# Performance work log

Measured on AMD Instinct MI355X. Metric: run time of the kernel, lower is better.

Reference implementation:

```python
import jax, jax.numpy as jnp
import numpy as np

B, T, D, H, A = 1, 262144, 8, 64, 4  # batch, seq_len, state_dim, hidden, n_actions


def setup_inputs() -> dict:
    key = jax.random.key(0)
    ks = jax.random.split(key, 10)
    s = lambda k, shape, sc: jax.random.normal(k, shape, dtype=jnp.float32) * sc
    return {
        "x": jax.random.normal(ks[0], (B, T, D), dtype=jnp.float32),
        # encoder MLP (Dense->tanh, Dense->tanh)
        "W1": s(ks[1], (D, H), 0.5), "b1": jnp.zeros((H,), jnp.float32),
        "W2": s(ks[2], (H, H), 0.15), "b2": jnp.zeros((H,), jnp.float32),
        # SimpleRNN params: h_t = tanh(x_t @ Wx + h_{t-1} @ Wh + b_rnn)
        "Wx": s(ks[3], (H, H), 0.15), "Wh": s(ks[4], (H, H), 0.1),
        "b_rnn": jnp.zeros((H,), jnp.float32),
        # means head
        "Wm": s(ks[5], (H, A), 0.01), "bm": jnp.zeros((A,), jnp.float32),
    }


def reference(x, W1, b1, W2, b2, Wx, Wh, b_rnn, Wm, bm):
    # Masking(mask_value=0): a timestep is masked if ALL features == 0
    mask = jnp.any(x != 0.0, axis=-1)  # [B, T] bool
    # TimeDistributed encoder (applies pointwise over time -> plain batched matmul)
    h1 = jnp.tanh(x @ W1 + b1)          # [B, T, H]
    h2 = jnp.tanh(h1 @ W2 + b2)         # [B, T, H]
    # Precompute input contribution to the RNN outside the scan (efficient form)
    xz = h2 @ Wx + b_rnn                # [B, T, H]

    def step(h, inp):
        z, m = inp                       # z: [B, H], m: [B]
        h_new = jnp.tanh(z + h @ Wh)
        # masked timesteps: carry previous state through (Keras RNN masking semantics)
        h = jnp.where(m[:, None], h_new, h)
        return h, h

    h0 = jnp.zeros((B, H), x.dtype)
    _, hs = jax.lax.scan(step, h0, (jnp.swapaxes(xz, 0, 1), jnp.swapaxes(mask, 0, 1)))
    hs = jnp.swapaxes(hs, 0, 1)          # [B, T, H]
    means = hs @ Wm + bm                 # [B, T, A]
    return means
```

## Files before the change

### kernel.cpp

```cpp
#include <hip/hip_runtime.h>
#include <hip/hip_bf16.h>

constexpr int T_LEN  = 262144;
constexpr int H      = 64;
constexpr int S_LEN  = 8;
constexpr int WARM   = 16;
constexpr int CHUNKS = T_LEN / S_LEN;
constexpr int NWAVE  = CHUNKS / 16;
constexpr int PRE_STRIDE = 68;
constexpr int ZPAD_TAIL = 4;

typedef __attribute__((ext_vector_type(8))) short short8;
typedef __attribute__((ext_vector_type(4))) float f32x4;

__device__ __forceinline__ float fast_tanh(float x) {
    float e = __expf(2.0f * x);
    return 1.0f - 2.0f * __builtin_amdgcn_rcpf(e + 1.0f);
}
__device__ __forceinline__ unsigned short f2bf(float v) {
    unsigned u = __builtin_bit_cast(unsigned, v);
    return (unsigned short)((u + 0x7fffu + ((u >> 16) & 1u)) >> 16);
}
__device__ __forceinline__ float bf2f(unsigned short b) {
    return __builtin_bit_cast(float, (unsigned)b << 16);
}
__device__ __forceinline__ unsigned pack2(float a, float b) {
#if __has_builtin(__builtin_amdgcn_cvt_pk_bf16_f32)
    typedef __attribute__((ext_vector_type(2))) __bf16 bf16x2;
    bf16x2 r = __builtin_amdgcn_cvt_pk_bf16_f32(a, b);
    return __builtin_bit_cast(unsigned, r);
#else
    return (unsigned)f2bf(a) | ((unsigned)f2bf(b) << 16);
#endif
}

__global__ __launch_bounds__(256) void encoder_kernel(
    const float* __restrict__ x,
    const float* __restrict__ W1, const float* __restrict__ b1,
    const float* __restrict__ W2, const float* __restrict__ b2,
    const float* __restrict__ Wx, const float* __restrict__ b_rnn,
    unsigned short* __restrict__ z_s, float* __restrict__ m_s)
{
    __shared__ uint4 w1f[4 * 64];
    __shared__ uint4 w2f[8 * 64];
    __shared__ uint4 w3f[8 * 64];
    __shared__ float pre_[4][16 * PRE_STRIDE];

    const int tid = threadIdx.x;
    const int w   = tid >> 6;
    const int l   = tid & 63;
    const int q   = l >> 4;
    const int l15 = l & 15;

    {
        const int n  = l;
        const int kg = w;
        float v2[16], v3[16];
        #pragma unroll
        for (int kk = 0; kk < 16; ++kk) {
            v2[kk] = W2[(kg * 16 + kk) * 64 + n];
            v3[kk] = Wx[(kg * 16 + kk) * 64 + n];
        }
        const int kh = kg >> 1;
        const int tn = n >> 4;
        #pragma unroll
        for (int s = 0; s < 2; ++s) {
            const int qq   = (2 * kg + s) & 3;
            const int lane = qq * 16 + (n & 15);
            uint4 o2, o3;
            o2.x = pack2(v2[s*8+0], v2[s*8+1]); o2.y = pack2(v2[s*8+2], v2[s*8+3]);
            o2.z = pack2(v2[s*8+4], v2[s*8+5]); o2.w = pack2(v2[s*8+6], v2[s*8+7]);
            o3.x = pack2(v3[s*8+0], v3[s*8+1]); o3.y = pack2(v3[s*8+2], v3[s*8+3]);
            o3.z = pack2(v3[s*8+4], v3[s*8+5]); o3.w = pack2(v3[s*8+6], v3[s*8+7]);
            w2f[(tn * 2 + kh) * 64 + lane] = o2;
            w3f[(tn * 2 + kh) * 64 + lane] = o3;
        }
        uint4 o1 = make_uint4(0, 0, 0, 0);
        if (q < 2) {
            float v1[8];
            #pragma unroll
            for (int j = 0; j < 8; ++j) v1[j] = W1[j * 64 + w * 16 + l15];
            o1.x = pack2(v1[0], v1[1]); o1.y = pack2(v1[2], v1[3]);
            o1.z = pack2(v1[4], v1[5]); o1.w = pack2(v1[6], v1[7]);
        }
        w1f[w * 64 + l] = o1;
    }
    __syncthreads();

    float b1v[4], b2v[4], brv[4];
    #pragma unroll
    for (int tn = 0; tn < 4; ++tn) {
        b1v[tn] = b1[tn * 16 + l15];
        b2v[tn] = b2[tn * 16 + l15];
        brv[tn] = b_rnn[tn * 16 + l15];
    }

    float* mypre = pre_[w];

    float4 xa = make_float4(0.f, 0.f, 0.f, 0.f), xb = xa;
    if (q < 2) {
        const size_t t0 = (size_t)(blockIdx.x * 256 + w * 16 + l15) * 8;
        xa = *(const float4*)(x + t0);
        xb = *(const float4*)(x + t0 + 4);
    }

    #pragma unroll
    for (int it = 0; it < 4; ++it) {
        const int t0w = blockIdx.x * 256 + it * 64 + w * 16;

        float4 na = xa, nb = xb;
        if (it < 3 && q < 2) {
            const size_t tn0 = (size_t)(t0w + 64 + l15) * 8;
            na = *(const float4*)(x + tn0);
            nb = *(const float4*)(x + tn0 + 4);
        }

        short8 a1 = (short8)0;
        if (q < 2) {
            const float xv[8] = {xa.x, xa.y, xa.z, xa.w, xb.x, xb.y, xb.z, xb.w};
            if (q == 0) {
                bool nz = false;
                #pragma unroll
                for (int d = 0; d < 8; ++d) nz = nz || (xv[d] != 0.0f);
                m_s[t0w + l15] = nz ? 1.0f : 0.0f;
                uint4 o;
                o.x = pack2(xv[0], xv[1]); o.y = pack2(xv[2], xv[3]);
                o.z = pack2(xv[4], xv[5]); o.w = pack2(xv[6], xv[7]);
                a1 = __builtin_bit_cast(short8, o);
            } else {
                float lo[8];
                #pragma unroll
                for (int d = 0; d < 8; ++d) lo[d] = xv[d] - bf2f(f2bf(xv[d]));
                uint4 o;
                o.x = pack2(lo[0], lo[1]); o.y = pack2(lo[2], lo[3]);
                o.z = pack2(lo[4], lo[5]); o.w = pack2(lo[6], lo[7]);
                a1 = __builtin_bit_cast(short8, o);
            }
        }

        {
            f32x4 acc[4];
            #pragma unroll
            for (int tn = 0; tn < 4; ++tn)
                acc[tn] = __builtin_amdgcn_mfma_f32_16x16x32_bf16(
                    a1, __builtin_bit_cast(short8, w1f[tn * 64 + l]),
                    (f32x4){0.f, 0.f, 0.f, 0.f}, 0, 0, 0);
            #pragma unroll
            for (int tn = 0; tn < 4; ++tn)
                #pragma unroll
                for (int r = 0; r < 4; ++r)
                    mypre[(q * 4 + r) * PRE_STRIDE + tn * 16 + l15] =
                        fast_tanh(acc[tn][r] + b1v[tn]);
        }
        __builtin_amdgcn_wave_barrier();

        short8 af[2];
        #pragma unroll
        for (int kh = 0; kh < 2; ++kh) {
            const uint4 r0 = *(const uint4*)(mypre + l15 * PRE_STRIDE + kh * 32 + q * 8);
            const uint4 r1 = *(const uint4*)(mypre + l15 * PRE_STRIDE + kh * 32 + q * 8 + 4);
            uint4 p;
            p.x = pack2(__builtin_bit_cast(float, r0.x), __builtin_bit_cast(float, r0.y));
            p.y = pack2(__builtin_bit_cast(float, r0.z), __builtin_bit_cast(float, r0.w));
            p.z = pack2(__builtin_bit_cast(float, r1.x), __builtin_bit_cast(float, r1.y));
            p.w = pack2(__builtin_bit_cast(float, r1.z), __builtin_bit_cast(float, r1.w));
            af[kh] = __builtin_bit_cast(short8, p);
        }
        __builtin_amdgcn_wave_barrier();

        {
            f32x4 acc[4];
            #pragma unroll
            for (int tn = 0; tn < 4; ++tn) {
                f32x4 d = {0.f, 0.f, 0.f, 0.f};
                d = __builtin_amdgcn_mfma_f32_16x16x32_bf16(
                        af[0], __builtin_bit_cast(short8, w2f[(tn * 2 + 0) * 64 + l]), d, 0, 0, 0);
                d = __builtin_amdgcn_mfma_f32_16x16x32_bf16(
                        af[1], __builtin_bit_cast(short8, w2f[(tn * 2 + 1) * 64 + l]), d, 0, 0, 0);
                acc[tn] = d;
            }
            #pragma unroll
            for (int tn = 0; tn < 4; ++tn)
                #pragma unroll
                for (int r = 0; r < 4; ++r)
                    mypre[(q * 4 + r) * PRE_STRIDE + tn * 16 + l15] =
                        fast_tanh(acc[tn][r] + b2v[tn]);
        }
        __builtin_amdgcn_wave_barrier();

        #pragma unroll
        for (int kh = 0; kh < 2; ++kh) {
            const uint4 r0 = *(const uint4*)(mypre + l15 * PRE_STRIDE + kh * 32 + q * 8);
            const uint4 r1 = *(const uint4*)(mypre + l15 * PRE_STRIDE + kh * 32 + q * 8 + 4);
            uint4 p;
            p.x = pack2(__builtin_bit_cast(float, r0.x), __builtin_bit_cast(float, r0.y));
            p.y = pack2(__builtin_bit_cast(float, r0.z), __builtin_bit_cast(float, r0.w));
            p.z = pack2(__builtin_bit_cast(float, r1.x), __builtin_bit_cast(float, r1.y));
            p.w = pack2(__builtin_bit_cast(float, r1.z), __builtin_bit_cast(float, r1.w));
            af[kh] = __builtin_bit_cast(short8, p);
        }
        __builtin_amdgcn_wave_barrier();

        {
            f32x4 acc[4];
            #pragma unroll
            for (int tn = 0; tn < 4; ++tn) {
                f32x4 d = {0.f, 0.f, 0.f, 0.f};
                d = __builtin_amdgcn_mfma_f32_16x16x32_bf16(
                        af[0], __builtin_bit_cast(short8, w3f[(tn * 2 + 0) * 64 + l]), d, 0, 0, 0);
                d = __builtin_amdgcn_mfma_f32_16x16x32_bf16(
                        af[1], __builtin_bit_cast(short8, w3f[(tn * 2 + 1) * 64 + l]), d, 0, 0, 0);
                acc[tn] = d;
            }
            #pragma unroll
            for (int tn = 0; tn < 4; ++tn)
                #pragma unroll
                for (int r = 0; r < 4; ++r)
                    mypre[(q * 4 + r) * PRE_STRIDE + tn * 16 + l15] = acc[tn][r] + brv[tn];
        }
        __builtin_amdgcn_wave_barrier();

        {
            const int ot = l >> 2;
            const int fq = l & 3;
            const float* src = mypre + ot * PRE_STRIDE + fq * 16;
            const uint4 r0 = *(const uint4*)(src + 0);
            const uint4 r1 = *(const uint4*)(src + 4);
            const uint4 r2 = *(const uint4*)(src + 8);
            const uint4 r3 = *(const uint4*)(src + 12);
            uint4 o0, o1;
            o0.x = pack2(__builtin_bit_cast(float, r0.x), __builtin_bit_cast(float, r0.y));
            o0.y = pack2(__builtin_bit_cast(float, r0.z), __builtin_bit_cast(float, r0.w));
            o0.z = pack2(__builtin_bit_cast(float, r1.x), __builtin_bit_cast(float, r1.y));
            o0.w = pack2(__builtin_bit_cast(float, r1.z), __builtin_bit_cast(float, r1.w));
            o1.x = pack2(__builtin_bit_cast(float, r2.x), __builtin_bit_cast(float, r2.y));
            o1.y = pack2(__builtin_bit_cast(float, r2.z), __builtin_bit_cast(float, r2.w));
            o1.z = pack2(__builtin_bit_cast(float, r3.x), __builtin_bit_cast(float, r3.y));
            o1.w = pack2(__builtin_bit_cast(float, r3.z), __builtin_bit_cast(float, r3.w));
            uint4* dst = (uint4*)(z_s + (size_t)(t0w + ot) * 64 + fq * 16);
            dst[0] = o0;
            dst[1] = o1;
        }
        __builtin_amdgcn_wave_barrier();

        xa = na; xb = nb;
    }
}

__global__ __launch_bounds__(256) void rnn_kernel(
    const unsigned short* __restrict__ z_pad, const float* __restrict__ m_pad,
    const float* __restrict__ Wh, const float* __restrict__ Wm,
    const float* __restrict__ bm, float* __restrict__ out)
{
    const int tid = threadIdx.x;
    const int w   = tid >> 6;
    const int l   = tid & 63;
    const int q   = l >> 4;
    const int n15 = l & 15;
    const int rw  = blockIdx.x * 4 + w;
    const int c   = rw * 16 + n15;

    short8 afrag[8];
    #pragma unroll
    for (int tn = 0; tn < 4; ++tn) {
        #pragma unroll
        for (int kh = 0; kh < 2; ++kh) {
            short8 s;
            #pragma unroll
            for (int j = 0; j < 8; ++j)
                s[j] = (short)f2bf(Wh[(kh * 32 + q * 8 + j) * 64 + tn * 16 + n15]);
            afrag[tn * 2 + kh] = s;
        }
    }
    short8 wmf[2];
    #pragma unroll
    for (int kh = 0; kh < 2; ++kh) {
        short8 s;
        #pragma unroll
        for (int j = 0; j < 8; ++j)
            s[j] = (n15 < 4) ? (short)f2bf(Wm[(kh * 32 + q * 8 + j) * 4 + n15]) : (short)0;
        wmf[kh] = s;
    }
    const float4 bmv = *(const float4*)bm;

    f32x4 hst[4];
    #pragma unroll
    for (int tn = 0; tn < 4; ++tn) hst[tn] = (f32x4){0.f, 0.f, 0.f, 0.f};
    short8 hB[2];
    hB[0] = (short8)0;
    hB[1] = (short8)0;

    const int idxA = ((2 * (q & 1) + 0) * 16 + n15) * 4;
    const int idxB = ((2 * (q & 1) + 1) * 16 + n15) * 4;
    const bool hiSel = (q >= 2);

    const unsigned short* zrow = z_pad + (size_t)c * S_LEN * 64;
    const float*          mrow = m_pad + (size_t)c * S_LEN;
    const int tneg = -(c * S_LEN);

    uint2 zb0[4], zb1[4];
    float mb0, mb1;
    #pragma unroll
    for (int tn = 0; tn < 4; ++tn) {
        zb0[tn] = *(const uint2*)(zrow + tn * 16 + q * 4);
        zb1[tn] = *(const uint2*)(zrow + 64 + tn * 16 + q * 4);
    }
    mb0 = mrow[0];
    mb1 = mrow[1];
    zrow += 128; mrow += 2;

    auto body = [&](uint2* zbuf, float& mref,
                    const unsigned short* zrl, const float* mrl,
                    int stv, bool means_prev, bool may_reset) {
        if (may_reset && rw == 0) {
            if (stv == tneg) {
                hB[0] = (short8)0; hB[1] = (short8)0;
                #pragma unroll
                for (int tn = 0; tn < 4; ++tn) hst[tn] = (f32x4){0.f, 0.f, 0.f, 0.f};
            }
        }
        f32x4 acc[4];
        #pragma unroll
        for (int mt = 0; mt < 4; ++mt) {
            f32x4 d = {0.f, 0.f, 0.f, 0.f};
            d = __builtin_amdgcn_mfma_f32_16x16x32_bf16(afrag[mt * 2 + 0], hB[0], d, 0, 0, 0);
            d = __builtin_amdgcn_mfma_f32_16x16x32_bf16(afrag[mt * 2 + 1], hB[1], d, 0, 0, 0);
            acc[mt] = d;
        }
        if (means_prev) {
            f32x4 a2 = {0.f, 0.f, 0.f, 0.f};
            a2 = __builtin_amdgcn_mfma_f32_16x16x32_bf16(wmf[0], hB[0], a2, 0, 0, 0);
            a2 = __builtin_amdgcn_mfma_f32_16x16x32_bf16(wmf[1], hB[1], a2, 0, 0, 0);
            if (q == 0) {
                const size_t tp = (size_t)c * S_LEN + (stv - 1);
                *(float4*)(out + tp * 4) =
                    make_float4(a2[0] + bmv.x, a2[1] + bmv.y, a2[2] + bmv.z, a2[3] + bmv.w);
            }
        }
        const bool upd = (mref != 0.0f);
        #pragma unroll
        for (int tn = 0; tn < 4; ++tn) {
            const unsigned short* zp = (const unsigned short*)&zbuf[tn];
            #pragma unroll
            for (int r = 0; r < 4; ++r) {
                const float nv = fast_tanh(acc[tn][r] + bf2f(zp[r]));
                hst[tn][r] = upd ? nv : hst[tn][r];
            }
        }
        unsigned P[4][2];
        #pragma unroll
        for (int tn = 0; tn < 4; ++tn) {
            P[tn][0] = pack2(hst[tn][0], hst[tn][1]);
            P[tn][1] = pack2(hst[tn][2], hst[tn][3]);
        }
        #pragma unroll
        for (int kh = 0; kh < 2; ++kh) {
            unsigned fd[4];
            #pragma unroll
            for (int d = 0; d < 4; ++d) {
                const int idx = (d < 2) ? idxA : idxB;
                const unsigned lo =
                    (unsigned)__builtin_amdgcn_ds_bpermute(idx, (int)P[2 * kh + 0][d & 1]);
                const unsigned hi =
                    (unsigned)__builtin_amdgcn_ds_bpermute(idx, (int)P[2 * kh + 1][d & 1]);
                fd[d] = hiSel ? hi : lo;
            }
            uint4 u = make_uint4(fd[0], fd[1], fd[2], fd[3]);
            hB[kh] = __builtin_bit_cast(short8, u);
        }
        #pragma unroll
        for (int tn = 0; tn < 4; ++tn)
            zbuf[tn] = *(const uint2*)(zrl + tn * 16 + q * 4);
        mref = mrl[0];
    };

    for (int i = 0; i < WARM / 2; ++i) {
        const int st = -WARM + 2 * i;
        body(zb0, mb0, zrow,      mrow,     st,     false, true);
        body(zb1, mb1, zrow + 64, mrow + 1, st + 1, false, true);
        zrow += 128; mrow += 2;
    }

    #pragma unroll
    for (int st = 0; st < S_LEN; ++st) {
        if ((st & 1) == 0)
            body(zb0, mb0, zrow + st * 64, mrow + st, st, st >= 1, st == 0);
        else
            body(zb1, mb1, zrow + st * 64, mrow + st, st, true, false);
    }

    {
        f32x4 a2 = {0.f, 0.f, 0.f, 0.f};
        a2 = __builtin_amdgcn_mfma_f32_16x16x32_bf16(wmf[0], hB[0], a2, 0, 0, 0);
        a2 = __builtin_amdgcn_mfma_f32_16x16x32_bf16(wmf[1], hB[1], a2, 0, 0, 0);
        if (q == 0) {
            const size_t tp = (size_t)c * S_LEN + (S_LEN - 1);
            *(float4*)(out + tp * 4) =
                make_float4(a2[0] + bmv.x, a2[1] + bmv.y, a2[2] + bmv.z, a2[3] + bmv.w);
        }
    }
}

extern "C" void kernel_launch(void* const* d_in, const int* in_sizes, int n_in,
                              void* d_out, int out_size, void* d_ws, size_t ws_size,
                              hipStream_t stream) {
    const float* x     = (const float*)d_in[0];
    const float* W1    = (const float*)d_in[1];
    const float* b1    = (const float*)d_in[2];
    const float* W2    = (const float*)d_in[3];
    const float* b2    = (const float*)d_in[4];
    const float* Wx    = (const float*)d_in[5];
    const float* Wh    = (const float*)d_in[6];
    const float* b_rnn = (const float*)d_in[7];
    const float* Wm    = (const float*)d_in[8];
    const float* bm    = (const float*)d_in[9];
    float* out = (float*)d_out;

    unsigned short* z_pad = (unsigned short*)d_ws;
    const size_t z_rows   = (size_t)(WARM + T_LEN + ZPAD_TAIL);
    float*          m_pad = (float*)((char*)d_ws + z_rows * H * 2);

    unsigned short* z_s = z_pad + (size_t)WARM * H;
    float*          m_s = m_pad + WARM;

    encoder_kernel<<<T_LEN / 256, 256, 0, stream>>>(x, W1, b1, W2, b2, Wx, b_rnn, z_s, m_s);
    rnn_kernel<<<NWAVE / 4, 256, 0, stream>>>(z_pad, m_pad, Wh, Wm, bm, out);
}
```

Measured before the change: 129.5 us.

## Permute Wh columns so MFMA output maps directly onto next-step B fragment

Reorders the columns of the recurrent weight fragments so that the MFMA accumulator layout of the new hidden state already matches the B-operand layout needed for the next step. This removes the per-step cross-lane ds_bpermute shuffles, the selects, and the separate fp32 hidden-state registers. The hidden state is now kept only in bf16, and the z loads use matching offsets. The serial recurrence loses its LDS-permute latency. In exchange, masked timesteps now carry over a bf16-rounded state rather than an fp32 state.

Result: no change. 129.9 us (+0.3%).

```diff
diff --git a/kernel.cpp b/kernel.cpp
--- a/kernel.cpp
+++ b/kernel.cpp
@@ -263,12 +263,13 @@
     short8 afrag[8];
     #pragma unroll
     for (int tn = 0; tn < 4; ++tn) {
+        const int prow = 32 * (tn >> 1) + 8 * (n15 >> 2) + 4 * (tn & 1) + (n15 & 3);
         #pragma unroll
         for (int kh = 0; kh < 2; ++kh) {
             short8 s;
             #pragma unroll
             for (int j = 0; j < 8; ++j)
-                s[j] = (short)f2bf(Wh[(kh * 32 + q * 8 + j) * 64 + tn * 16 + n15]);
+                s[j] = (short)f2bf(Wh[(kh * 32 + q * 8 + j) * 64 + prow]);
             afrag[tn * 2 + kh] = s;
         }
     }
@@ -283,27 +284,30 @@
     }
     const float4 bmv = *(const float4*)bm;
 
-    f32x4 hst[4];
-    #pragma unroll
-    for (int tn = 0; tn < 4; ++tn) hst[tn] = (f32x4){0.f, 0.f, 0.f, 0.f};
     short8 hB[2];
     hB[0] = (short8)0;
     hB[1] = (short8)0;
 
-    const int idxA = ((2 * (q & 1) + 0) * 16 + n15) * 4;
-    const int idxB = ((2 * (q & 1) + 1) * 16 + n15) * 4;
-    const bool hiSel = (q >= 2);
-
     const unsigned short* zrow = z_pad + (size_t)c * S_LEN * 64;
     const float*          mrow = m_pad + (size_t)c * S_LEN;
     const int tneg = -(c * S_LEN);
 
+    const int zo0 = 8 * q;
+    const int zo1 = 8 * q + 4;
+    const int zo2 = 8 * q + 32;
+    const int zo3 = 8 * q + 36;
+
     uint2 zb0[4], zb1[4];
     float mb0, mb1;
-    #pragma unroll
-    for (int tn = 0; tn < 4; ++tn) {
-        zb0[tn] = *(const uint2*)(zrow + tn * 16 + q * 4);
-        zb1[tn] = *(const uint2*)(zrow + 64 + tn * 16 + q * 4);
+    {
+        zb0[0] = *(const uint2*)(zrow + zo0);
+        zb0[1] = *(const uint2*)(zrow + zo1);
+        zb0[2] = *(const uint2*)(zrow + zo2);
+        zb0[3] = *(const uint2*)(zrow + zo3);
+        zb1[0] = *(const uint2*)(zrow + 64 + zo0);
+        zb1[1] = *(const uint2*)(zrow + 64 + zo1);
+        zb1[2] = *(const uint2*)(zrow + 64 + zo2);
+        zb1[3] = *(const uint2*)(zrow + 64 + zo3);
     }
     mb0 = mrow[0];
     mb1 = mrow[1];
@@ -315,8 +319,6 @@
         if (may_reset && rw == 0) {
             if (stv == tneg) {
                 hB[0] = (short8)0; hB[1] = (short8)0;
-                #pragma unroll
-                for (int tn = 0; tn < 4; ++tn) hst[tn] = (f32x4){0.f, 0.f, 0.f, 0.f};
             }
         }
         f32x4 acc[4];
@@ -341,36 +343,21 @@
         #pragma unroll
         for (int tn = 0; tn < 4; ++tn) {
             const unsigned short* zp = (const unsigned short*)&zbuf[tn];
-            #pragma unroll
-            for (int r = 0; r < 4; ++r) {
-                const float nv = fast_tanh(acc[tn][r] + bf2f(zp[r]));
-                hst[tn][r] = upd ? nv : hst[tn][r];
-            }
-        }
-        unsigned P[4][2];
-        #pragma unroll
-        for (int tn = 0; tn < 4; ++tn) {
-            P[tn][0] = pack2(hst[tn][0], hst[tn][1]);
-            P[tn][1] = pack2(hst[tn][2], hst[tn][3]);
-        }
-        #pragma unroll
-        for (int kh = 0; kh < 2; ++kh) {
-            unsigned fd[4];
-            #pragma unroll
-            for (int d = 0; d < 4; ++d) {
-                const int idx = (d < 2) ? idxA : idxB;
-                const unsigned lo =
-                    (unsigned)__builtin_amdgcn_ds_bpermute(idx, (int)P[2 * kh + 0][d & 1]);
-                const unsigned hi =
-                    (unsigned)__builtin_amdgcn_ds_bpermute(idx, (int)P[2 * kh + 1][d & 1]);
-                fd[d] = hiSel ? hi : lo;
-            }
-            uint4 u = make_uint4(fd[0], fd[1], fd[2], fd[3]);
-            hB[kh] = __builtin_bit_cast(short8, u);
-        }
-        #pragma unroll
-        for (int tn = 0; tn < 4; ++tn)
-            zbuf[tn] = *(const uint2*)(zrl + tn * 16 + q * 4);
+            float th[4];
+            #pragma unroll
+            for (int r = 0; r < 4; ++r)
+                th[r] = fast_tanh(acc[tn][r] + bf2f(zp[r]));
+            const unsigned w0 = pack2(th[0], th[1]);
+            const unsigned w1 = pack2(th[2], th[3]);
+            unsigned* hw = (unsigned*)&hB[tn >> 1];
+            const int wi = (tn & 1) * 2;
+            hw[wi + 0] = upd ? w0 : hw[wi + 0];
+            hw[wi + 1] = upd ? w1 : hw[wi + 1];
+        }
+        zbuf[0] = *(const uint2*)(zrl + zo0);
+        zbuf[1] = *(const uint2*)(zrl + zo1);
+        zbuf[2] = *(const uint2*)(zrl + zo2);
+        zbuf[3] = *(const uint2*)(zrl + zo3);
         mref = mrl[0];
     };
 
```
